# Kernel tuning notes

Measured on AMD Instinct MI355X. Metric: run time of the kernel, lower is better.

Reference implementation:

```python
import jax, jax.numpy as jnp
import numpy as np

D_MODEL = 1024
NUM_HEADS = 16
D_HEAD = D_MODEL // NUM_HEADS
THETA = 10000.0


def _rope_tables(seq_len, d_k, theta):
    # inv_powers_k = theta**(-(2k-2)/d_k) for k=1..d_k/2 == theta**(-arange(0,d_k,2)/d_k)
    inv_powers = theta ** (-jnp.arange(0, d_k, 2, dtype=jnp.float32) / d_k)  # [d_k/2]
    positions = jnp.arange(seq_len, dtype=jnp.float32)
    angles = jnp.outer(positions, inv_powers)  # [S, d_k/2]
    return jnp.cos(angles), jnp.sin(angles)


def _apply_rope(x, cos, sin):
    # x: [..., S, d_k]; cos/sin: [S, d_k/2] broadcast over leading dims
    x_even = x[..., 0::2]
    x_odd = x[..., 1::2]
    r_even = x_even * cos - x_odd * sin
    r_odd = x_even * sin + x_odd * cos
    # interleave back: [..., S, d_k/2, 2] -> [..., S, d_k]
    return jnp.stack([r_even, r_odd], axis=-1).reshape(x.shape)


def setup_inputs() -> dict:
    key = jax.random.key(0)
    ks = jax.random.split(key, 5)
    B, S = 2, 2048
    sigma = (2.0 / (D_MODEL + D_MODEL)) ** 0.5
    x = jax.random.normal(ks[0], (B, S, D_MODEL), dtype=jnp.float32)
    wq = jax.random.normal(ks[1], (D_MODEL, D_MODEL), dtype=jnp.float32) * sigma
    wk = jax.random.normal(ks[2], (D_MODEL, D_MODEL), dtype=jnp.float32) * sigma
    wv = jax.random.normal(ks[3], (D_MODEL, D_MODEL), dtype=jnp.float32) * sigma
    wo = jax.random.normal(ks[4], (D_MODEL, D_MODEL), dtype=jnp.float32) * sigma
    return {"x": x, "wq": wq, "wk": wk, "wv": wv, "wo": wo}


def reference(x, wq, wk, wv, wo):
    B, S, D = x.shape
    H, Dh = NUM_HEADS, D_HEAD
    # Linear: einx.dot('... in, out in -> ... out') == x @ W.T
    q = jnp.einsum('bsd,od->bso', x, wq)
    k = jnp.einsum('bsd,od->bso', x, wk)
    v = jnp.einsum('bsd,od->bso', x, wv)
    # split heads: [B, S, H, Dh] -> [B, H, S, Dh]
    q = q.reshape(B, S, H, Dh).transpose(0, 2, 1, 3)
    k = k.reshape(B, S, H, Dh).transpose(0, 2, 1, 3)
    v = v.reshape(B, S, H, Dh).transpose(0, 2, 1, 3)
    cos, sin = _rope_tables(S, Dh, THETA)
    q = _apply_rope(q, cos, sin)
    k = _apply_rope(k, cos, sin)
    scale = 1.0 / jnp.sqrt(jnp.float32(Dh))
    scores = jnp.einsum('bhqd,bhkd->bhqk', q, k) * scale  # [B,H,S,S]
    causal = jnp.tril(jnp.ones((S, S), dtype=bool))
    scores = jnp.where(causal, scores, -jnp.inf)
    probs = jax.nn.softmax(scores, axis=-1)
    attn = jnp.einsum('bhqk,bhkd->bhqd', probs, v)
    attn = attn.transpose(0, 2, 1, 3).reshape(B, S, D)
    return jnp.einsum('bsd,od->bso', attn, wo)
```

## Files before the change

### kernel.cpp

```cpp
#include <hip/hip_runtime.h>
#include <hip/hip_bf16.h>
#include <math.h>

#define B_SZ   2
#define SEQ    2048
#define DM     1024
#define NH     16
#define DH     64
#define MROWS  (B_SZ * SEQ)
#define DQKV   (3 * DM)

typedef __attribute__((ext_vector_type(8))) short short8;
typedef __attribute__((ext_vector_type(4))) float f32x4;
typedef __attribute__((ext_vector_type(16))) float f32x16;
typedef __attribute__((ext_vector_type(4))) unsigned short us4;
typedef __attribute__((ext_vector_type(2))) unsigned int u32x2;

__device__ __forceinline__ float b2f(unsigned short u) {
    union { float f; unsigned int i; } x; x.i = ((unsigned int)u) << 16; return x.f;
}
__device__ __forceinline__ unsigned short f2b(float f) {
    union { float f; unsigned int i; } x; x.f = f;
    return (unsigned short)((x.i + 0x7fffu + ((x.i >> 16) & 1u)) >> 16);
}
__device__ __forceinline__ unsigned int pk2b(float a, float b) {
    float2 f2; f2.x = a; f2.y = b;
    __hip_bfloat162 hb = __float22bfloat162_rn(f2);
    return *reinterpret_cast<unsigned int*>(&hb);
}
__device__ __forceinline__ float fexp2(float x) {
    float r; asm("v_exp_f32 %0, %1" : "=v"(r) : "v"(x)); return r;
}
__device__ __forceinline__ void swap32(unsigned int& a, unsigned int& b) {
    asm("v_permlane32_swap_b32 %0, %1" : "+v"(a), "+v"(b));
}

__device__ __forceinline__ void gload_lds16(const unsigned short* g, unsigned short* lds_base_uniform) {
    __builtin_amdgcn_global_load_lds(
        (const __attribute__((address_space(1))) unsigned int*)g,
        (__attribute__((address_space(3))) unsigned int*)lds_base_uniform,
        16, 0, 0);
}

#define NX4 (MROWS * DM / 4)
#define NW4 (DM * DM / 4)

__global__ __launch_bounds__(256) void cvt_all(const float* __restrict__ x,
                                               const float* __restrict__ wq,
                                               const float* __restrict__ wk,
                                               const float* __restrict__ wv,
                                               const float* __restrict__ wo,
                                               unsigned short* __restrict__ xb,
                                               unsigned short* __restrict__ wqkv,
                                               unsigned short* __restrict__ wob,
                                               float* __restrict__ tab) {
    const int i = blockIdx.x * 256 + threadIdx.x;
    const int ncvt = NX4 + 4 * NW4;
    if (i < ncvt) {
        const float* src; unsigned short* dst; int off;
        if (i < NX4) { src = x; dst = xb; off = i; }
        else {
            int j = i - NX4;
            int w = j >> 18;
            off = j & (NW4 - 1);
            src = (w == 0) ? wq : (w == 1) ? wk : (w == 2) ? wv : wo;
            dst = (w < 3) ? wqkv + (size_t)w * DM * DM : wob;
        }
        float4 v = reinterpret_cast<const float4*>(src)[off];
        us4 o = { f2b(v.x), f2b(v.y), f2b(v.z), f2b(v.w) };
        reinterpret_cast<us4*>(dst)[off] = o;
    } else {
        int t = i - ncvt;
        if (t < SEQ * 32) {
            int s = t >> 5, fi = t & 31;
            float inv = powf(10000.0f, -(float)fi / 32.0f);
            float ang = (float)s * inv;
            tab[2 * t]     = cosf(ang);
            tab[2 * t + 1] = sinf(ang);
        }
    }
}

#define BM 128
#define BN 128
#define BK 32

__global__ __launch_bounds__(256, 2) void gemm_out(const unsigned short* __restrict__ A,
                                                   const unsigned short* __restrict__ B,
                                                   float* __restrict__ Cout) {
    __shared__ unsigned short As[3][128 * BK];
    __shared__ unsigned short Bs[3][64 * BK];
    const int tid  = threadIdx.x;
    const int lane = tid & 63, wid = tid >> 6;
    const int lm = lane & 15, lg = lane >> 4;
    const int brow = blockIdx.y * 128, bcol = blockIdx.x * 64;
    const int K = DM, N = DM;
    const int NT = K / BK;

    f32x4 acc[2][4] = {};

    const int rA  = tid >> 2;
    const int kc8 = (tid & 3) * 8;
    const unsigned short* gA0 = A + (size_t)(brow + rA) * K + kc8;
    const unsigned short* gA1 = A + (size_t)(brow + 64 + rA) * K + kc8;
    const unsigned short* gB0 = B + (size_t)(bcol + rA) * K + kc8;
    const int la = wid * 512;

#define OSTAGE(t, bi)                                        \
    {                                                        \
        const int _o = (t) * BK;                             \
        gload_lds16(gA0 + _o, &As[bi][la]);                  \
        gload_lds16(gA1 + _o, &As[bi][2048 + la]);           \
        gload_lds16(gB0 + _o, &Bs[bi][la]);                  \
    }

    OSTAGE(0, 0);
    OSTAGE(1, 1);
    asm volatile("s_waitcnt vmcnt(3)" ::: "memory");
    __builtin_amdgcn_s_barrier();
    asm volatile("" ::: "memory");

    int cb = 0, sb = 2;
    for (int k = 0; k < NT; ++k) {
        if (k + 2 < NT) OSTAGE(k + 2, sb);
        short8 a[2], b[4];
#pragma unroll
        for (int m = 0; m < 2; ++m)
            a[m] = *reinterpret_cast<const short8*>(&As[cb][(wid * 32 + m * 16 + lm) * BK + lg * 8]);
#pragma unroll
        for (int n = 0; n < 4; ++n)
            b[n] = *reinterpret_cast<const short8*>(&Bs[cb][(n * 16 + lm) * BK + lg * 8]);
#pragma unroll
        for (int m = 0; m < 2; ++m)
#pragma unroll
            for (int n = 0; n < 4; ++n)
                acc[m][n] = __builtin_amdgcn_mfma_f32_16x16x32_bf16(a[m], b[n], acc[m][n], 0, 0, 0);
        if (k + 1 < NT) {
            if (k + 2 < NT) asm volatile("s_waitcnt vmcnt(3)" ::: "memory");
            else            asm volatile("s_waitcnt vmcnt(0)" ::: "memory");
            __builtin_amdgcn_s_barrier();
            asm volatile("" ::: "memory");
        }
        cb = (cb == 2) ? 0 : cb + 1;
        sb = (sb == 2) ? 0 : sb + 1;
    }
#undef OSTAGE

#pragma unroll
    for (int m = 0; m < 2; ++m) {
#pragma unroll
        for (int r = 0; r < 4; ++r) {
            const size_t base = (size_t)(brow + wid * 32 + m * 16 + lg * 4 + r) * N + bcol + lm;
#pragma unroll
            for (int n = 0; n < 4; ++n)
                Cout[base + n * 16] = acc[m][n][r];
        }
    }
}

__global__ __launch_bounds__(256, 2) void gemm_qkv(const unsigned short* __restrict__ A,
                                                   const unsigned short* __restrict__ B,
                                                   unsigned short* __restrict__ qkv,
                                                   unsigned short* __restrict__ vT,
                                                   const float* __restrict__ tab) {
    __shared__ unsigned short As[3][BM * BK];
    __shared__ unsigned short Bs[3][BN * BK];
    const int tid  = threadIdx.x;
    const int lane = tid & 63, wid = tid >> 6;
    const int wr = wid >> 1, wc = wid & 1;
    const int lm = lane & 15, lg = lane >> 4;
    const int brow = blockIdx.y * BM, bcol = blockIdx.x * BN;
    const int K = DM;
    const int NT = K / BK;

    f32x4 acc[4][4] = {};

    const int rA  = tid >> 2;
    const int kc8 = (tid & 3) * 8;
    const unsigned short* gA0 = A + (size_t)(brow + rA) * K + kc8;
    const unsigned short* gA1 = A + (size_t)(brow + 64 + rA) * K + kc8;
    const unsigned short* gB0 = B + (size_t)(bcol + rA) * K + kc8;
    const unsigned short* gB1 = B + (size_t)(bcol + 64 + rA) * K + kc8;
    const int la = wid * 512;

#define QSTAGE(t, bi)                                        \
    {                                                        \
        const int _o = (t) * BK;                             \
        gload_lds16(gA0 + _o, &As[bi][la]);                  \
        gload_lds16(gA1 + _o, &As[bi][2048 + la]);           \
        gload_lds16(gB0 + _o, &Bs[bi][la]);                  \
        gload_lds16(gB1 + _o, &Bs[bi][2048 + la]);           \
    }

    QSTAGE(0, 0);
    QSTAGE(1, 1);
    asm volatile("s_waitcnt vmcnt(4)" ::: "memory");
    __builtin_amdgcn_s_barrier();
    asm volatile("" ::: "memory");

    int cb = 0, sb = 2;
    for (int k = 0; k < NT; ++k) {
        if (k + 2 < NT) QSTAGE(k + 2, sb);
        short8 a[4], b[4];
#pragma unroll
        for (int m = 0; m < 4; ++m)
            a[m] = *reinterpret_cast<const short8*>(&As[cb][(wr * 64 + m * 16 + lm) * BK + lg * 8]);
#pragma unroll
        for (int n = 0; n < 4; ++n)
            b[n] = *reinterpret_cast<const short8*>(&Bs[cb][(wc * 64 + n * 16 + lm) * BK + lg * 8]);
#pragma unroll
        for (int m = 0; m < 4; ++m)
#pragma unroll
            for (int n = 0; n < 4; ++n)
                acc[m][n] = __builtin_amdgcn_mfma_f32_16x16x32_bf16(a[m], b[n], acc[m][n], 0, 0, 0);
        if (k + 1 < NT) {
            if (k + 2 < NT) asm volatile("s_waitcnt vmcnt(4)" ::: "memory");
            else            asm volatile("s_waitcnt vmcnt(0)" ::: "memory");
            __builtin_amdgcn_s_barrier();
            asm volatile("" ::: "memory");
        }
        cb = (cb == 2) ? 0 : cb + 1;
        sb = (sb == 2) ? 0 : sb + 1;
    }
#undef QSTAGE

    const int reg = blockIdx.x >> 3;
    if (reg < 2) {
        const float qs = (reg == 0) ? (0.125f * 1.4426950408889634f) : 1.0f;
        const int odd = lm & 1;
#pragma unroll
        for (int m = 0; m < 4; ++m) {
#pragma unroll
            for (int r = 0; r < 4; ++r) {
                const int row = brow + wr * 64 + m * 16 + lg * 4 + r;
                const int s   = row & (SEQ - 1);
                const size_t base = (size_t)row * DQKV + bcol + wc * 64 + lm;
#pragma unroll
                for (int n = 0; n < 4; ++n) {
                    float v  = acc[m][n][r];
                    float pv = __shfl_xor(v, 1);
                    const int fi = (n * 16 + lm) >> 1;
                    float2 cs = reinterpret_cast<const float2*>(tab)[s * 32 + fi];
                    float c = cs.x * qs, sn = cs.y * qs;
                    float out = odd ? (pv * sn + v * c) : (v * c - pv * sn);
                    qkv[base + n * 16] = f2b(out);
                }
            }
        }
    } else {
        const int b = brow >> 11;
#pragma unroll
        for (int m = 0; m < 4; ++m) {
            const int s0 = (brow + wr * 64 + m * 16 + lg * 4) & (SEQ - 1);
#pragma unroll
            for (int n = 0; n < 4; ++n) {
                const int vcol = bcol + wc * 64 + n * 16 + lm - 2 * DM;
                const int h = vcol >> 6, d = vcol & 63;
                us4 val = { f2b(acc[m][n][0]), f2b(acc[m][n][1]),
                            f2b(acc[m][n][2]), f2b(acc[m][n][3]) };
                *reinterpret_cast<us4*>(vT + (size_t)((b * NH + h) * DH + d) * SEQ + s0) = val;
            }
        }
    }
}

__global__ __launch_bounds__(256, 4) void attn_mfma(const unsigned short* __restrict__ qkv,
                                                    const unsigned short* __restrict__ vT,
                                                    unsigned short* __restrict__ o) {
    const int tid  = threadIdx.x;
    const int wid  = tid >> 6;
    const int lane = tid & 63;
    const int l31 = lane & 31, lo = lane >> 5;
    const int tile = wid >> 1;
    const int half = wid & 1;

    const int bid = blockIdx.x;
    const int u   = bid >> 3;
    const int j   = u & 31;
    const int bh_hi = u >> 5;
    const int chunk = (bh_hi & 1) ? (31 - j) : j;
    const int bh = (bid & 7) + 8 * bh_hi;
    const int b = bh >> 4, h = bh & 15;
    const int qbase = chunk * 64 + tile * 32;
    const int nb = chunk + 1;

    __shared__ unsigned short Kl[2][4096];
    __shared__ unsigned short Vl[2][4096];

    const unsigned short* kb = qkv + ((size_t)b * SEQ) * DQKV + DM + h * DH;
    const unsigned short* vb = vT + ((size_t)bh) * DH * SEQ;

    const int pr  = tid >> 4;
    const int st  = tid & 15;
    const int c16 = st ^ pr;
    const int hf  = c16 >> 3;
    const int cc  = c16 & 7;
    const unsigned short* kst0 = kb + (size_t)(pr + hf * 32) * DQKV + cc * 8;
    const unsigned short* kst1 = kst0 + (size_t)16 * DQKV;
    const unsigned short* vst0 = vb + (size_t)(pr + hf * 32) * SEQ + cc * 8;
    const unsigned short* vst1 = vst0 + 16 * SEQ;
    const int sdst = wid * 512;

    const unsigned short* qr = qkv + ((size_t)(b * SEQ + qbase + l31)) * DQKV + h * DH + lo * 8;
    short8 qb4[4];
#pragma unroll
    for (int dc = 0; dc < 4; ++dc)
        qb4[dc] = *reinterpret_cast<const short8*>(qr + dc * 16);

    f32x16 oA = {0,0,0,0,0,0,0,0,0,0,0,0,0,0,0,0};
    f32x16 oB = {0,0,0,0,0,0,0,0,0,0,0,0,0,0,0,0};
    float mrun = -3.0e38f, lrun = 0.f;

    gload_lds16(kst0, &Kl[0][sdst]);
    gload_lds16(kst1, &Kl[0][2048 + sdst]);
    gload_lds16(vst0, &Vl[0][sdst]);
    gload_lds16(vst1, &Vl[0][2048 + sdst]);
    __syncthreads();

    const int lx = l31 & 15;
    int buf = 0;
    for (int blk = 0; blk < nb; ++blk) {
        const int kbase = blk << 6;

        if (blk + 1 < nb) {
            const size_t ko = (size_t)(kbase + 64) * DQKV;
            const int    vo = kbase + 64;
            gload_lds16(kst0 + ko, &Kl[buf ^ 1][sdst]);
            gload_lds16(kst1 + ko, &Kl[buf ^ 1][2048 + sdst]);
            gload_lds16(vst0 + vo, &Vl[buf ^ 1][sdst]);
            gload_lds16(vst1 + vo, &Vl[buf ^ 1][2048 + sdst]);
        }

        const char* Kb = (const char*)&Kl[buf][0];
        const char* Vb = (const char*)&Vl[buf][0];

        f32x16 S = {0,0,0,0,0,0,0,0,0,0,0,0,0,0,0,0};
        __builtin_amdgcn_s_setprio(1);
#pragma unroll
        for (int dc = 0; dc < 4; ++dc) {
            const int ss = ((half * 8 + dc * 2 + lo) ^ lx) << 4;
            short8 k0 = *reinterpret_cast<const short8*>(Kb + l31 * 256 + ss);
            S = __builtin_amdgcn_mfma_f32_32x32x16_bf16(k0, qb4[dc], S, 0, 0, 0);
        }
        __builtin_amdgcn_s_setprio(0);

        short8 vf[2][2];
#pragma unroll
        for (int kc = 0; kc < 2; ++kc) {
#pragma unroll
            for (int dh = 0; dh < 2; ++dh) {
                const int sts = ((dh * 8 + (half * 2 + kc) * 2 + lo) ^ lx) << 4;
                vf[kc][dh] = *reinterpret_cast<const short8*>(Vb + l31 * 256 + sts);
            }
        }

        float s[16];
#pragma unroll
        for (int r = 0; r < 16; ++r) s[r] = S[r];

        if (blk == nb - 1) {
            const int q = qbase + l31;
#pragma unroll
            for (int r = 0; r < 16; ++r) {
                const int kk = kbase + half * 32 + (r & 3) + 8 * (r >> 2) + 4 * lo;
                s[r] = (kk <= q) ? s[r] : -INFINITY;
            }
        }

        float t0 = fmaxf(s[0], s[1]),  t1 = fmaxf(s[2], s[3]);
        float t2 = fmaxf(s[4], s[5]),  t3 = fmaxf(s[6], s[7]);
        float t4 = fmaxf(s[8], s[9]),  t5 = fmaxf(s[10], s[11]);
        float t6 = fmaxf(s[12], s[13]), t7 = fmaxf(s[14], s[15]);
        float lmax = fmaxf(fmaxf(fmaxf(t0, t1), fmaxf(t2, t3)),
                           fmaxf(fmaxf(t4, t5), fmaxf(t6, t7)));

        if (!__all(lmax - mrun <= 8.0f)) {
            float mx = fmaxf(lmax, __shfl_xor(lmax, 32));
            float mn = fmaxf(mrun, mx);
            float fsc = fexp2(mrun - mn);
            mrun = mn;
            lrun *= fsc;
#pragma unroll
            for (int r = 0; r < 16; ++r) {
                float fr = __shfl(fsc, (r & 3) + 8 * (r >> 2) + 4 * lo);
                oA[r] *= fr; oB[r] *= fr;
            }
        }

#pragma unroll
        for (int r = 0; r < 16; ++r) s[r] = fexp2(s[r] - mrun);

        float a0 = (s[0] + s[1]) + (s[2] + s[3]);
        float a1 = (s[4] + s[5]) + (s[6] + s[7]);
        float a2 = (s[8] + s[9]) + (s[10] + s[11]);
        float a3 = (s[12] + s[13]) + (s[14] + s[15]);
        float ps = (a0 + a1) + (a2 + a3);
        ps += __shfl_xor(ps, 32);
        lrun += ps;

        unsigned int pf[2][4];
        {
            unsigned int a0u = pk2b(s[0], s[1]);
            unsigned int b0u = pk2b(s[4], s[5]);
            swap32(a0u, b0u);
            unsigned int a1u = pk2b(s[2], s[3]);
            unsigned int b1u = pk2b(s[6], s[7]);
            swap32(a1u, b1u);
            pf[0][0] = a0u; pf[0][1] = a1u; pf[0][2] = b0u; pf[0][3] = b1u;
            unsigned int a2u = pk2b(s[8], s[9]);
            unsigned int b2u = pk2b(s[12], s[13]);
            swap32(a2u, b2u);
            unsigned int a3u = pk2b(s[10], s[11]);
            unsigned int b3u = pk2b(s[14], s[15]);
            swap32(a3u, b3u);
            pf[1][0] = a2u; pf[1][1] = a3u; pf[1][2] = b2u; pf[1][3] = b3u;
        }

        __builtin_amdgcn_s_setprio(1);
#pragma unroll
        for (int kc = 0; kc < 2; ++kc) {
            union { unsigned int u[4]; short8 v; } P;
            P.u[0] = pf[kc][0]; P.u[1] = pf[kc][1]; P.u[2] = pf[kc][2]; P.u[3] = pf[kc][3];
            oA = __builtin_amdgcn_mfma_f32_32x32x16_bf16(P.v, vf[kc][0], oA, 0, 0, 0);
            oB = __builtin_amdgcn_mfma_f32_32x32x16_bf16(P.v, vf[kc][1], oB, 0, 0, 0);
        }
        __builtin_amdgcn_s_setprio(0);

        __syncthreads();
        buf ^= 1;
    }

    float* mbase = (tile == 0) ? (float*)&Kl[0][0] : (float*)&Vl[0][0];
    if (half == 0) {
#pragma unroll
        for (int g = 0; g < 8; ++g) {
            f32x4 w;
#pragma unroll
            for (int t = 0; t < 4; ++t)
                w[t] = (g < 4) ? oA[(g & 3) * 4 + t] : oB[(g & 3) * 4 + t];
            *reinterpret_cast<f32x4*>(mbase + lane * 32 + ((g ^ (lane & 7)) * 4)) = w;
        }
        if (lo == 0) {
            mbase[2048 + l31 * 2]     = mrun;
            mbase[2048 + l31 * 2 + 1] = lrun;
        }
    }
    __syncthreads();
    if (half == 1) {
        const float m0 = mbase[2048 + l31 * 2];
        const float l0 = mbase[2048 + l31 * 2 + 1];
        const float ms = fmaxf(m0, mrun);
        const float f0 = fexp2(m0 - ms);
        const float f1 = fexp2(mrun - ms);
        const float li = 1.0f / (l0 * f0 + lrun * f1);
#pragma unroll
        for (int g = 0; g < 8; ++g) {
            f32x4 rd = *reinterpret_cast<const f32x4*>(mbase + lane * 32 + ((g ^ (lane & 7)) * 4));
#pragma unroll
            for (int t = 0; t < 4; ++t) {
                const int r = (g & 3) * 4 + t;
                const float mine = (g < 4) ? oA[r] : oB[r];
                const int qr2 = (r & 3) + 8 * (r >> 2) + 4 * lo;
                const float f0q = __shfl(f0, qr2);
                const float f1q = __shfl(f1, qr2);
                const float liq = __shfl(li, qr2);
                const float val = (rd[t] * f0q + mine * f1q) * liq;
                const size_t rowoff = ((size_t)(b * SEQ + qbase + qr2)) * DM + h * DH + ((g < 4) ? 0 : 32);
                o[rowoff + l31] = f2b(val);
            }
        }
    }
}

extern "C" void kernel_launch(void* const* d_in, const int* in_sizes, int n_in,
                              void* d_out, int out_size, void* d_ws, size_t ws_size,
                              hipStream_t stream) {
    const float* x  = (const float*)d_in[0];
    const float* wq = (const float*)d_in[1];
    const float* wk = (const float*)d_in[2];
    const float* wv = (const float*)d_in[3];
    const float* wo = (const float*)d_in[4];
    float* out = (float*)d_out;

    char* ws = (char*)d_ws;
    const size_t MB = 1024 * 1024;
    unsigned short* xb      = (unsigned short*)(ws);
    unsigned short* wqkv    = (unsigned short*)(ws + 8 * MB);
    unsigned short* wob     = (unsigned short*)(ws + 14 * MB);
    unsigned short* qkv     = (unsigned short*)(ws + 16 * MB);
    unsigned short* vT      = (unsigned short*)(ws + 40 * MB);
    float*          ropetab = (float*)(ws + 48 * MB);
    unsigned short* attn_bf = xb;

    const int cvt_grid = (NX4 + 4 * NW4 + SEQ * 32) / 256;
    cvt_all<<<cvt_grid, 256, 0, stream>>>(x, wq, wk, wv, wo, xb, wqkv, wob, ropetab);

    gemm_qkv<<<dim3(DQKV / BN, MROWS / BM), 256, 0, stream>>>(xb, wqkv, qkv, vT, ropetab);

    attn_mfma<<<1024, 256, 0, stream>>>(qkv, vT, attn_bf);

    gemm_out<<<dim3(DM / 64, MROWS / 128), 256, 0, stream>>>(attn_bf, wob, out);
}
```

Before: 112.8 us.

## Enlarge attention blocks to 128 queries with 512 threads sharing K/V tiles

The attention kernel now runs 512 threads per block covering 128 query rows instead of 64, so each staged K/V tile in LDS is reused by four query tiles rather than two. The grid is halved and the chunk-reversal mapping is adjusted for 16 chunks. Each thread now issues one async load per buffer instead of two, and causal masking covers the last two key blocks. The merge scratch moves into a dedicated shared array. The change cuts global K/V traffic per query but reduces block count and may cost occupancy, since larger blocks need more LDS and registers.

New measurement: 114.7 us. No clear change (+1.7%).

```diff
diff --git a/kernel.cpp b/kernel.cpp
--- a/kernel.cpp
+++ b/kernel.cpp
@@ -264,7 +264,7 @@
     }
 }
 
-__global__ __launch_bounds__(256, 4) void attn_mfma(const unsigned short* __restrict__ qkv,
+__global__ __launch_bounds__(512, 4) void attn_mfma(const unsigned short* __restrict__ qkv,
                                                     const unsigned short* __restrict__ vT,
                                                     unsigned short* __restrict__ o) {
     const int tid  = threadIdx.x;
@@ -276,29 +276,28 @@
 
     const int bid = blockIdx.x;
     const int u   = bid >> 3;
-    const int j   = u & 31;
-    const int bh_hi = u >> 5;
-    const int chunk = (bh_hi & 1) ? (31 - j) : j;
+    const int j   = u & 15;
+    const int bh_hi = u >> 4;
+    const int chunk = ((u >> 5) & 1) ? (15 - j) : j;
     const int bh = (bid & 7) + 8 * bh_hi;
     const int b = bh >> 4, h = bh & 15;
-    const int qbase = chunk * 64 + tile * 32;
-    const int nb = chunk + 1;
+    const int qbase = chunk * 128 + tile * 32;
+    const int nb = 2 * chunk + 2;
 
     __shared__ unsigned short Kl[2][4096];
     __shared__ unsigned short Vl[2][4096];
+    __shared__ float Ml[4][64];
 
     const unsigned short* kb = qkv + ((size_t)b * SEQ) * DQKV + DM + h * DH;
     const unsigned short* vb = vT + ((size_t)bh) * DH * SEQ;
 
     const int pr  = tid >> 4;
     const int st  = tid & 15;
-    const int c16 = st ^ pr;
+    const int c16 = st ^ (pr & 15);
     const int hf  = c16 >> 3;
     const int cc  = c16 & 7;
-    const unsigned short* kst0 = kb + (size_t)(pr + hf * 32) * DQKV + cc * 8;
-    const unsigned short* kst1 = kst0 + (size_t)16 * DQKV;
-    const unsigned short* vst0 = vb + (size_t)(pr + hf * 32) * SEQ + cc * 8;
-    const unsigned short* vst1 = vst0 + 16 * SEQ;
+    const unsigned short* kst = kb + (size_t)(pr + hf * 32) * DQKV + cc * 8;
+    const unsigned short* vst = vb + (size_t)(pr + hf * 32) * SEQ + cc * 8;
     const int sdst = wid * 512;
 
     const unsigned short* qr = qkv + ((size_t)(b * SEQ + qbase + l31)) * DQKV + h * DH + lo * 8;
@@ -311,10 +310,8 @@
     f32x16 oB = {0,0,0,0,0,0,0,0,0,0,0,0,0,0,0,0};
     float mrun = -3.0e38f, lrun = 0.f;
 
-    gload_lds16(kst0, &Kl[0][sdst]);
-    gload_lds16(kst1, &Kl[0][2048 + sdst]);
-    gload_lds16(vst0, &Vl[0][sdst]);
-    gload_lds16(vst1, &Vl[0][2048 + sdst]);
+    gload_lds16(kst, &Kl[0][sdst]);
+    gload_lds16(vst, &Vl[0][sdst]);
     __syncthreads();
 
     const int lx = l31 & 15;
@@ -323,12 +320,8 @@
         const int kbase = blk << 6;
 
         if (blk + 1 < nb) {
-            const size_t ko = (size_t)(kbase + 64) * DQKV;
-            const int    vo = kbase + 64;
-            gload_lds16(kst0 + ko, &Kl[buf ^ 1][sdst]);
-            gload_lds16(kst1 + ko, &Kl[buf ^ 1][2048 + sdst]);
-            gload_lds16(vst0 + vo, &Vl[buf ^ 1][sdst]);
-            gload_lds16(vst1 + vo, &Vl[buf ^ 1][2048 + sdst]);
+            gload_lds16(kst + (size_t)(kbase + 64) * DQKV, &Kl[buf ^ 1][sdst]);
+            gload_lds16(vst + (kbase + 64),                &Vl[buf ^ 1][sdst]);
         }
 
         const char* Kb = (const char*)&Kl[buf][0];
@@ -358,7 +351,7 @@
 #pragma unroll
         for (int r = 0; r < 16; ++r) s[r] = S[r];
 
-        if (blk == nb - 1) {
+        if (blk + 2 >= nb) {
             const int q = qbase + l31;
 #pragma unroll
             for (int r = 0; r < 16; ++r) {
@@ -430,7 +423,9 @@
         buf ^= 1;
     }
 
-    float* mbase = (tile == 0) ? (float*)&Kl[0][0] : (float*)&Vl[0][0];
+    float* mbase = (tile == 0) ? (float*)&Kl[0][0] :
+                   (tile == 1) ? (float*)&Kl[1][0] :
+                   (tile == 2) ? (float*)&Vl[0][0] : (float*)&Vl[1][0];
     if (half == 0) {
 #pragma unroll
         for (int g = 0; g < 8; ++g) {
@@ -441,14 +436,14 @@
             *reinterpret_cast<f32x4*>(mbase + lane * 32 + ((g ^ (lane & 7)) * 4)) = w;
         }
         if (lo == 0) {
-            mbase[2048 + l31 * 2]     = mrun;
-            mbase[2048 + l31 * 2 + 1] = lrun;
+            Ml[tile][l31 * 2]     = mrun;
+            Ml[tile][l31 * 2 + 1] = lrun;
         }
     }
     __syncthreads();
     if (half == 1) {
-        const float m0 = mbase[2048 + l31 * 2];
-        const float l0 = mbase[2048 + l31 * 2 + 1];
+        const float m0 = Ml[tile][l31 * 2];
+        const float l0 = Ml[tile][l31 * 2 + 1];
         const float ms = fmaxf(m0, mrun);
         const float f0 = fexp2(m0 - ms);
         const float f1 = fexp2(mrun - ms);
@@ -497,7 +492,7 @@
 
     gemm_qkv<<<dim3(DQKV / BN, MROWS / BM), 256, 0, stream>>>(xb, wqkv, qkv, vT, ropetab);
 
-    attn_mfma<<<1024, 256, 0, stream>>>(qkv, vT, attn_bf);
+    attn_mfma<<<512, 512, 0, stream>>>(qkv, vT, attn_bf);
 
     gemm_out<<<dim3(DM / 64, MROWS / 128), 256, 0, stream>>>(attn_bf, wob, out);
 }
```

## Split causal attention KV range across two blocks and merge partials

Applied to the files above, without the earlier changes.

Each query chunk's KV blocks are now divided into two halves processed by separate workgroups, doubling the grid to 2048 blocks. Each half writes unnormalized bf16 partial outputs plus per-row max and sum to workspace. A new merge kernel then combines the two halves with log-sum-exp rescaling. The aim is to shorten the longest causal chunks and balance load across CUs, at the cost of an extra launch, extra global traffic for the partials, and bf16 rounding of unnormalized partials.

After: 117.6 us. +4.2%, slower.

```diff
diff --git a/kernel.cpp b/kernel.cpp
--- a/kernel.cpp
+++ b/kernel.cpp
@@ -266,7 +266,9 @@
 
 __global__ __launch_bounds__(256, 4) void attn_mfma(const unsigned short* __restrict__ qkv,
                                                     const unsigned short* __restrict__ vT,
-                                                    unsigned short* __restrict__ o) {
+                                                    unsigned short* __restrict__ P0,
+                                                    unsigned short* __restrict__ P1,
+                                                    float* __restrict__ ML) {
     const int tid  = threadIdx.x;
     const int wid  = tid >> 6;
     const int lane = tid & 63;
@@ -274,15 +276,22 @@
     const int tile = wid >> 1;
     const int half = wid & 1;
 
-    const int bid = blockIdx.x;
-    const int u   = bid >> 3;
-    const int j   = u & 31;
+    const int bid  = blockIdx.x;
+    const int xcd  = bid & 7;
+    const int r2   = bid >> 3;
+    const int split = r2 & 1;
+    const int u    = r2 >> 1;
+    const int j    = u & 31;
     const int bh_hi = u >> 5;
     const int chunk = (bh_hi & 1) ? (31 - j) : j;
-    const int bh = (bid & 7) + 8 * bh_hi;
+    const int bh = xcd + 8 * bh_hi;
     const int b = bh >> 4, h = bh & 15;
     const int qbase = chunk * 64 + tile * 32;
-    const int nb = chunk + 1;
+
+    const int nb_total = chunk + 1;
+    const int nhalf = (nb_total + 1) >> 1;
+    const int t0 = split ? nhalf : 0;
+    const int t1 = split ? nb_total : nhalf;
 
     __shared__ unsigned short Kl[2][4096];
     __shared__ unsigned short Vl[2][4096];
@@ -311,18 +320,22 @@
     f32x16 oB = {0,0,0,0,0,0,0,0,0,0,0,0,0,0,0,0};
     float mrun = -3.0e38f, lrun = 0.f;
 
-    gload_lds16(kst0, &Kl[0][sdst]);
-    gload_lds16(kst1, &Kl[0][2048 + sdst]);
-    gload_lds16(vst0, &Vl[0][sdst]);
-    gload_lds16(vst1, &Vl[0][2048 + sdst]);
+    {
+        const size_t pk0 = (size_t)(t0 << 6) * DQKV;
+        const int    pv0 = t0 << 6;
+        gload_lds16(kst0 + pk0, &Kl[0][sdst]);
+        gload_lds16(kst1 + pk0, &Kl[0][2048 + sdst]);
+        gload_lds16(vst0 + pv0, &Vl[0][sdst]);
+        gload_lds16(vst1 + pv0, &Vl[0][2048 + sdst]);
+    }
     __syncthreads();
 
     const int lx = l31 & 15;
     int buf = 0;
-    for (int blk = 0; blk < nb; ++blk) {
+    for (int blk = t0; blk < t1; ++blk) {
         const int kbase = blk << 6;
 
-        if (blk + 1 < nb) {
+        if (blk + 1 < t1) {
             const size_t ko = (size_t)(kbase + 64) * DQKV;
             const int    vo = kbase + 64;
             gload_lds16(kst0 + ko, &Kl[buf ^ 1][sdst]);
@@ -358,7 +371,7 @@
 #pragma unroll
         for (int r = 0; r < 16; ++r) s[r] = S[r];
 
-        if (blk == nb - 1) {
+        if (blk == chunk) {
             const int q = qbase + l31;
 #pragma unroll
             for (int r = 0; r < 16; ++r) {
@@ -367,12 +380,12 @@
             }
         }
 
-        float t0 = fmaxf(s[0], s[1]),  t1 = fmaxf(s[2], s[3]);
-        float t2 = fmaxf(s[4], s[5]),  t3 = fmaxf(s[6], s[7]);
-        float t4 = fmaxf(s[8], s[9]),  t5 = fmaxf(s[10], s[11]);
-        float t6 = fmaxf(s[12], s[13]), t7 = fmaxf(s[14], s[15]);
-        float lmax = fmaxf(fmaxf(fmaxf(t0, t1), fmaxf(t2, t3)),
-                           fmaxf(fmaxf(t4, t5), fmaxf(t6, t7)));
+        float t0m = fmaxf(s[0], s[1]),  t1m = fmaxf(s[2], s[3]);
+        float t2m = fmaxf(s[4], s[5]),  t3m = fmaxf(s[6], s[7]);
+        float t4m = fmaxf(s[8], s[9]),  t5m = fmaxf(s[10], s[11]);
+        float t6m = fmaxf(s[12], s[13]), t7m = fmaxf(s[14], s[15]);
+        float lmax = fmaxf(fmaxf(fmaxf(t0m, t1m), fmaxf(t2m, t3m)),
+                           fmaxf(fmaxf(t4m, t5m), fmaxf(t6m, t7m)));
 
         if (!__all(lmax - mrun <= 8.0f)) {
             float mx = fmaxf(lmax, __shfl_xor(lmax, 32));
@@ -447,12 +460,21 @@
     }
     __syncthreads();
     if (half == 1) {
+        unsigned short* pO = split ? P1 : P0;
+        float* Mp = ML + (size_t)split * 131072;
+        float* Lp = Mp + 65536;
+
         const float m0 = mbase[2048 + l31 * 2];
         const float l0 = mbase[2048 + l31 * 2 + 1];
         const float ms = fmaxf(m0, mrun);
         const float f0 = fexp2(m0 - ms);
         const float f1 = fexp2(mrun - ms);
-        const float li = 1.0f / (l0 * f0 + lrun * f1);
+        const float lp = l0 * f0 + lrun * f1;
+        if (lo == 0) {
+            const int mi = (b * SEQ + qbase + l31) * 16 + h;
+            Mp[mi] = ms;
+            Lp[mi] = lp;
+        }
 #pragma unroll
         for (int g = 0; g < 8; ++g) {
             f32x4 rd = *reinterpret_cast<const f32x4*>(mbase + lane * 32 + ((g ^ (lane & 7)) * 4));
@@ -463,13 +485,45 @@
                 const int qr2 = (r & 3) + 8 * (r >> 2) + 4 * lo;
                 const float f0q = __shfl(f0, qr2);
                 const float f1q = __shfl(f1, qr2);
-                const float liq = __shfl(li, qr2);
-                const float val = (rd[t] * f0q + mine * f1q) * liq;
+                const float val = rd[t] * f0q + mine * f1q;
                 const size_t rowoff = ((size_t)(b * SEQ + qbase + qr2)) * DM + h * DH + ((g < 4) ? 0 : 32);
-                o[rowoff + l31] = f2b(val);
+                pO[rowoff + l31] = f2b(val);
             }
         }
     }
+}
+
+__global__ __launch_bounds__(256) void attn_merge(const unsigned short* __restrict__ P0,
+                                                  const unsigned short* __restrict__ P1,
+                                                  const float* __restrict__ ML,
+                                                  unsigned short* __restrict__ out) {
+    const int idx = blockIdx.x * 256 + threadIdx.x;
+    const int rh = idx >> 3;
+    const int d0 = (idx & 7) * 8;
+    const int row = rh >> 4, h = rh & 15;
+
+    const float m0 = ML[rh];
+    const float l0 = ML[65536 + rh];
+    const float m1 = ML[131072 + rh];
+    const float l1 = ML[196608 + rh];
+    const float ms = fmaxf(m0, m1);
+    const float f0 = fexp2(m0 - ms);
+    const float f1 = fexp2(m1 - ms);
+    const float li = 1.0f / (l0 * f0 + l1 * f1);
+
+    const size_t base = (size_t)row * DM + h * DH + d0;
+    us4 a0 = *reinterpret_cast<const us4*>(P0 + base);
+    us4 a1 = *reinterpret_cast<const us4*>(P0 + base + 4);
+    us4 c0 = *reinterpret_cast<const us4*>(P1 + base);
+    us4 c1 = *reinterpret_cast<const us4*>(P1 + base + 4);
+    us4 o0v, o1v;
+#pragma unroll
+    for (int t = 0; t < 4; ++t) {
+        o0v[t] = f2b((b2f(a0[t]) * f0 + b2f(c0[t]) * f1) * li);
+        o1v[t] = f2b((b2f(a1[t]) * f0 + b2f(c1[t]) * f1) * li);
+    }
+    *reinterpret_cast<us4*>(out + base)     = o0v;
+    *reinterpret_cast<us4*>(out + base + 4) = o1v;
 }
 
 extern "C" void kernel_launch(void* const* d_in, const int* in_sizes, int n_in,
@@ -490,14 +544,19 @@
     unsigned short* qkv     = (unsigned short*)(ws + 16 * MB);
     unsigned short* vT      = (unsigned short*)(ws + 40 * MB);
     float*          ropetab = (float*)(ws + 48 * MB);
-    unsigned short* attn_bf = xb;
+    unsigned short* P0      = xb;
+    unsigned short* P1      = (unsigned short*)(ws + 48 * MB);
+    float*          ML      = (float*)(ws + 56 * MB);
+    unsigned short* attn_bf = P0;
 
     const int cvt_grid = (NX4 + 4 * NW4 + SEQ * 32) / 256;
     cvt_all<<<cvt_grid, 256, 0, stream>>>(x, wq, wk, wv, wo, xb, wqkv, wob, ropetab);
 
     gemm_qkv<<<dim3(DQKV / BN, MROWS / BM), 256, 0, stream>>>(xb, wqkv, qkv, vT, ropetab);
 
-    attn_mfma<<<1024, 256, 0, stream>>>(qkv, vT, attn_bf);
+    attn_mfma<<<2048, 256, 0, stream>>>(qkv, vT, P0, P1, ML);
+
+    attn_merge<<<2048, 256, 0, stream>>>(P0, P1, ML, attn_bf);
 
     gemm_out<<<dim3(DM / 64, MROWS / 128), 256, 0, stream>>>(attn_bf, wob, out);
 }
```
